# Optimization experiments

Measured on AMD Instinct MI355X. Metric: run time of the kernel, lower is better.

## Reference

```python
import jax, jax.numpy as jnp
import numpy as np
import math

N_HEADS = 12


def setup_inputs() -> dict:
    key = jax.random.key(0)
    ks = jax.random.split(key, 6)
    B, S, DIM = 4, 2048, 768
    h = jax.random.normal(ks[0], (B, S, DIM), dtype=jnp.float32)
    attn_mask = jnp.ones((B, 1, 1, S), dtype=jnp.int32)
    scale = 1.0 / math.sqrt(DIM)
    wq = jax.random.normal(ks[1], (DIM, DIM), dtype=jnp.float32) * scale
    wk = jax.random.normal(ks[2], (DIM, DIM), dtype=jnp.float32) * scale
    wv = jax.random.normal(ks[3], (DIM, DIM), dtype=jnp.float32) * scale
    wo = jax.random.normal(ks[4], (DIM, DIM), dtype=jnp.float32) * scale
    return {"h": h, "attn_mask": attn_mask, "wq": wq, "wk": wk, "wv": wv, "wo": wo}


def reference(h, attn_mask, wq, wk, wv, wo):
    B, S, dim = h.shape
    H = N_HEADS
    D = dim // H
    qk_scale = 1.0 / math.sqrt(D)
    # NOTE: original uses .view(B, H, S, D) on the [B, S, H*D] projection —
    # a raw reshape, NOT the usual (B,S,H,D)->(B,H,S,D) transpose. Reproduce exactly.
    hq = (h @ wq.T).reshape(B, H, S, D)
    hk = (h @ wk.T).reshape(B, H, S, D)
    hv = (h @ wv.T).reshape(B, H, S, D)
    scores = jnp.einsum("bhqd,bhkd->bhqk", hq, hk) * qk_scale  # [B,H,S,S]
    scores = jnp.where(attn_mask == 0, -jnp.inf, scores)
    attn = jax.nn.softmax(scores.astype(jnp.float32), axis=-1)
    ctx = jnp.einsum("bhqk,bhkd->bhqd", attn, hv)  # [B,H,S,D]
    # dropout is identity in eval mode
    ctx = ctx.reshape(B, S, H * D)
    return ctx @ wo.T
```

## Files before the change

### kernel.cpp

```cpp
#include <hip/hip_runtime.h>
#include <math.h>

typedef __bf16 bf16x8 __attribute__((ext_vector_type(8)));
typedef float  f32x4  __attribute__((ext_vector_type(4)));
typedef float  f32x16 __attribute__((ext_vector_type(16)));

#define MFMA16(a, b, c) __builtin_amdgcn_mfma_f32_16x16x32_bf16((a), (b), (c), 0, 0, 0)
#define MFMA32(a, b, c) __builtin_amdgcn_mfma_f32_32x32x16_bf16((a), (b), (c), 0, 0, 0)

__device__ __forceinline__ unsigned short f2bf(float f) {
    unsigned int u = __float_as_uint(f);
    u += 0x7fffu + ((u >> 16) & 1u);
    return (unsigned short)(u >> 16);
}

__device__ __forceinline__ void gll16(const unsigned short* g, unsigned short* l) {
    __builtin_amdgcn_global_load_lds(
        (const __attribute__((address_space(1))) unsigned int*)g,
        (__attribute__((address_space(3))) unsigned int*)l, 16, 0, 0);
}

__global__ __launch_bounds__(256) void convert_kernel(
    const float* __restrict__ h, const float* __restrict__ wq,
    const float* __restrict__ wk, const float* __restrict__ wv,
    const float* __restrict__ wo,
    unsigned short* __restrict__ hb, unsigned short* __restrict__ wb)
{
    const int NH4 = 1572864;
    const int NW4 = 147456;
    int i4 = blockIdx.x * 256 + threadIdx.x;
    const float4* src;
    unsigned short* dst;
    int off;
    float sc = 1.0f;
    if (i4 < NH4) {
        src = (const float4*)h; dst = hb; off = i4;
    } else {
        int j = i4 - NH4;
        int w = j / NW4;
        off = j - w * NW4;
        const float* s = (w == 0) ? wq : (w == 1) ? wk : (w == 2) ? wv : wo;
        if (w == 0) sc = 0.18033688011112042f;
        src = (const float4*)s;
        dst = wb + w * 589824;
    }
    float4 v = src[off];
    ushort4 o;
    o.x = f2bf(v.x * sc); o.y = f2bf(v.y * sc);
    o.z = f2bf(v.z * sc); o.w = f2bf(v.w * sc);
    ((ushort4*)dst)[off] = o;
}

template <typename OutT>
__global__ __launch_bounds__(256) void gemm_bt(
    const unsigned short* __restrict__ A,
    const unsigned short* __restrict__ Bm,
    OutT* __restrict__ C)
{
    constexpr int K = 768, N = 768;
    __shared__ unsigned short As[2][128 * 32];
    __shared__ unsigned short Bs[2][128 * 32];
    const unsigned short* Bz = Bm + (size_t)blockIdx.z * N * K;
    OutT* Cz = C + (size_t)blockIdx.z * 8192 * N;

    const int tid  = threadIdx.x;
    const int bm   = blockIdx.x * 128, bn = blockIdx.y * 128;
    const int wave = tid >> 6, lane = tid & 63;
    const int wm   = (wave & 1) * 64, wn = (wave >> 1) * 64;
    const int l16  = lane & 15, quad = lane >> 4;

    const int sr  = tid >> 2;
    const int sp8 = ((tid & 3) ^ (sr & 3)) * 8;
    const int slot8 = (quad ^ (l16 & 3)) * 8;

    auto stage = [&](int k0, int bi) {
        gll16(A  + (size_t)(bm + sr) * K      + k0 + sp8, As[bi] + tid * 8);
        gll16(A  + (size_t)(bm + 64 + sr) * K + k0 + sp8, As[bi] + 2048 + tid * 8);
        gll16(Bz + (size_t)(bn + sr) * K      + k0 + sp8, Bs[bi] + tid * 8);
        gll16(Bz + (size_t)(bn + 64 + sr) * K + k0 + sp8, Bs[bi] + 2048 + tid * 8);
    };

    f32x4 acc[4][4] = {};

    stage(0, 0);
    __syncthreads();

    for (int i = 0; i < 24; i++) {
        const int cur = i & 1;
        if (i < 23) stage((i + 1) * 32, cur ^ 1);

        bf16x8 af[4], bfv[4];
        #pragma unroll
        for (int ii = 0; ii < 4; ii++)
            af[ii] = *(const bf16x8*)(As[cur] + (wm + ii * 16 + l16) * 32 + slot8);
        #pragma unroll
        for (int jj = 0; jj < 4; jj++)
            bfv[jj] = *(const bf16x8*)(Bs[cur] + (wn + jj * 16 + l16) * 32 + slot8);
        #pragma unroll
        for (int ii = 0; ii < 4; ii++)
            #pragma unroll
            for (int jj = 0; jj < 4; jj++)
                acc[ii][jj] = MFMA16(af[ii], bfv[jj], acc[ii][jj]);

        __syncthreads();
    }

    #pragma unroll
    for (int ii = 0; ii < 4; ii++) {
        #pragma unroll
        for (int jj = 0; jj < 4; jj++) {
            int row0 = bm + wm + ii * 16 + quad * 4;
            int col  = bn + wn + jj * 16 + l16;
            #pragma unroll
            for (int r = 0; r < 4; r++) {
                float v = acc[ii][jj][r];
                size_t idx = (size_t)(row0 + r) * N + col;
                if constexpr (sizeof(OutT) == 2) Cz[idx] = f2bf(v);
                else                             Cz[idx] = v;
            }
        }
    }
}

__global__ __launch_bounds__(256) void vtrans_kernel(
    const unsigned short* __restrict__ Vg,
    unsigned short* __restrict__ vt)
{
    constexpr int LDT = 72;
    __shared__ unsigned short Ts[64 * LDT];
    const int b = blockIdx.z, hh = blockIdx.y, kp0 = blockIdx.x * 64;
    const int tid = threadIdx.x;
    const size_t boff = (size_t)b * (24576 * 64);
    const int rowV0 = hh * 2048 + kp0;

    #pragma unroll
    for (int rep = 0; rep < 2; rep++) {
        int idx = rep * 256 + tid;
        int r = idx >> 3, dp = (idx & 7) * 8;
        uint4 v = *(const uint4*)(Vg + boff + (size_t)(rowV0 + r) * 64 + dp);
        unsigned short tmp[8];
        *(uint4*)tmp = v;
        #pragma unroll
        for (int i = 0; i < 8; i++) Ts[(dp + i) * LDT + r] = tmp[i];
    }
    __syncthreads();
    unsigned short* vtb = vt + ((size_t)(b * 12 + hh)) * 64 * 2048;
    #pragma unroll
    for (int rep = 0; rep < 2; rep++) {
        int idx = rep * 256 + tid;
        int d = idx >> 3, kp = (idx & 7) * 8;
        uint4 v = *(const uint4*)(Ts + d * LDT + kp);
        *(uint4*)(vtb + (size_t)d * 2048 + kp0 + kp) = v;
    }
}

__global__ __launch_bounds__(256) void attn_kernel(
    const unsigned short* __restrict__ Qg,
    const unsigned short* __restrict__ Kg,
    const unsigned short* __restrict__ vt,
    const int* __restrict__ mask,
    unsigned short* __restrict__ Og)
{
    __shared__ unsigned short Ks[3 * 2048];
    __shared__ unsigned short Vs[3 * 2048];
    __shared__ unsigned long long msh[32];

    const int b = blockIdx.z, hh = blockIdx.y, qt = blockIdx.x;
    const int tid  = threadIdx.x;
    const int wave = tid >> 6, lane = tid & 63;
    const int c31  = lane & 31, h = lane >> 5;
    const size_t boff = (size_t)b * (24576 * 64);
    const int rowQ0 = hh * 2048 + qt * 128;
    const int rowK0 = hh * 2048;
    const unsigned short* vtg = vt + ((size_t)(b * 12 + hh)) * 64 * 2048;
    const int swk = c31 & 7;
    const int swv = c31 & 3;

    const int srowK = tid >> 3;
    const int schK  = ((tid & 7) ^ (srowK & 7)) * 8;
    const int srowV = tid >> 2;
    const int schV  = ((tid & 3) ^ (srowV & 3)) * 8;

    auto stageKV = [&](int kt, int bi) {
        gll16(Kg  + boff + (size_t)(rowK0 + kt * 32 + srowK) * 64 + schK,
              Ks + bi * 2048 + tid * 8);
        gll16(vtg + (size_t)srowV * 2048 + kt * 32 + schV,
              Vs + bi * 2048 + tid * 8);
    };

    bf16x8 qf[4];
    {
        const unsigned short* qrow =
            Qg + boff + (size_t)(rowQ0 + wave * 32 + c31) * 64;
        #pragma unroll
        for (int c = 0; c < 4; c++)
            qf[c] = *(const bf16x8*)(qrow + (2 * c + h) * 8);
    }

    {
        const int4 a = *(const int4*)(mask + b * 2048 + tid * 8);
        const int4 c = *(const int4*)(mask + b * 2048 + tid * 8 + 4);
        unsigned char byte =
            (a.x != 0 ? 1u : 0u)       | (a.y != 0 ? 2u : 0u) |
            (a.z != 0 ? 4u : 0u)       | (a.w != 0 ? 8u : 0u) |
            (c.x != 0 ? 16u : 0u)      | (c.y != 0 ? 32u : 0u) |
            (c.z != 0 ? 64u : 0u)      | (c.w != 0 ? 128u : 0u);
        ((unsigned char*)msh)[tid] = byte;
    }
    __syncthreads();

    stageKV(0, 0);
    stageKV(1, 1);

    f32x16 acc[2] = {};
    f32x16 acc_l  = {};
    bf16x8 onesf;
    #pragma unroll
    for (int i = 0; i < 8; i++) onesf[i] = (__bf16)1.0f;

    int cur = 0;
    for (int kt = 0; kt < 64; kt++) {
        if (kt < 63) asm volatile("s_waitcnt vmcnt(2)\n\ts_barrier" ::: "memory");
        else         asm volatile("s_waitcnt vmcnt(0)\n\ts_barrier" ::: "memory");
        __builtin_amdgcn_sched_barrier(0);

        if (kt < 62) {
            int nb = cur + 2; if (nb >= 3) nb -= 3;
            stageKV(kt + 2, nb);
        }

        const unsigned int am = ((const unsigned int*)msh)[kt];
        const unsigned short* Kc = Ks + cur * 2048;
        const unsigned short* Vc = Vs + cur * 2048;

        f32x16 sT;
        {
            f32x16 z = {};
            __builtin_amdgcn_s_setprio(1);
            #pragma unroll
            for (int c = 0; c < 4; c++) {
                int ch = (2 * c + h) ^ swk;
                bf16x8 kf = *(const bf16x8*)(Kc + c31 * 64 + ch * 8);
                z = MFMA32(kf, qf[c], z);
            }
            __builtin_amdgcn_s_setprio(0);
            sT = z;
        }

        unsigned int p01[4], p23[4];
        if (am == 0xFFFFFFFFu) {
            #pragma unroll
            for (int s = 0; s < 4; s++) {
                float e0 = __builtin_amdgcn_exp2f(sT[4*s+0]);
                float e1 = __builtin_amdgcn_exp2f(sT[4*s+1]);
                float e2 = __builtin_amdgcn_exp2f(sT[4*s+2]);
                float e3 = __builtin_amdgcn_exp2f(sT[4*s+3]);
                asm("v_cvt_pk_bf16_f32 %0, %1, %2"
                    : "=v"(p01[s]) : "v"(e0), "v"(e1));
                asm("v_cvt_pk_bf16_f32 %0, %1, %2"
                    : "=v"(p23[s]) : "v"(e2), "v"(e3));
            }
        } else {
            #pragma unroll
            for (int s = 0; s < 4; s++) {
                unsigned int nib = (am >> (8 * s + 4 * h)) & 0xFu;
                float e0 = __builtin_amdgcn_exp2f(sT[4*s+0]);
                float e1 = __builtin_amdgcn_exp2f(sT[4*s+1]);
                float e2 = __builtin_amdgcn_exp2f(sT[4*s+2]);
                float e3 = __builtin_amdgcn_exp2f(sT[4*s+3]);
                e0 = (nib & 1u) ? e0 : 0.f;
                e1 = (nib & 2u) ? e1 : 0.f;
                e2 = (nib & 4u) ? e2 : 0.f;
                e3 = (nib & 8u) ? e3 : 0.f;
                asm("v_cvt_pk_bf16_f32 %0, %1, %2"
                    : "=v"(p01[s]) : "v"(e0), "v"(e1));
                asm("v_cvt_pk_bf16_f32 %0, %1, %2"
                    : "=v"(p23[s]) : "v"(e2), "v"(e3));
            }
        }

        __builtin_amdgcn_s_setprio(1);
        #pragma unroll
        for (int kc = 0; kc < 2; kc++) {
            unsigned int a01 = p01[2 * kc], b01 = p01[2 * kc + 1];
            unsigned int a23 = p23[2 * kc], b23 = p23[2 * kc + 1];
            asm("v_permlane32_swap_b32 %0, %1" : "+v"(a01), "+v"(b01));
            asm("v_permlane32_swap_b32 %0, %1" : "+v"(a23), "+v"(b23));
            uint4 pfu;
            pfu.x = a01;
            pfu.y = a23;
            pfu.z = b01;
            pfu.w = b23;
            bf16x8 pf;
            __builtin_memcpy(&pf, &pfu, 16);
            #pragma unroll
            for (int nt = 0; nt < 2; nt++) {
                int chv = (2 * kc + h) ^ swv;
                bf16x8 vf = *(const bf16x8*)(Vc + (nt * 32 + c31) * 32 + chv * 8);
                acc[nt] = MFMA32(pf, vf, acc[nt]);
            }
            acc_l = MFMA32(pf, onesf, acc_l);
        }
        __builtin_amdgcn_s_setprio(0);

        cur = (cur == 2) ? 0 : cur + 1;
    }

    #pragma unroll
    for (int reg = 0; reg < 16; reg++) {
        int rowfn = (reg & 3) + 8 * (reg >> 2) + 4 * h;
        float li = __builtin_amdgcn_rcpf(acc_l[reg]);
        int row = rowQ0 + wave * 32 + rowfn;
        #pragma unroll
        for (int nt = 0; nt < 2; nt++)
            Og[boff + (size_t)row * 64 + nt * 32 + c31] = f2bf(acc[nt][reg] * li);
    }
}

extern "C" void kernel_launch(void* const* d_in, const int* in_sizes, int n_in,
                              void* d_out, int out_size, void* d_ws, size_t ws_size,
                              hipStream_t stream)
{
    const float* h    = (const float*)d_in[0];
    const int*   mask = (const int*)d_in[1];
    const float* wq   = (const float*)d_in[2];
    const float* wk   = (const float*)d_in[3];
    const float* wv   = (const float*)d_in[4];
    const float* wo   = (const float*)d_in[5];

    unsigned short* hb  = (unsigned short*)d_ws;
    unsigned short* wb  = hb + 6291456;
    unsigned short* qkv = wb + 4 * 589824;
    unsigned short* ctx = qkv + (size_t)3 * 6291456;

    convert_kernel<<<8448, 256, 0, stream>>>(h, wq, wk, wv, wo, hb, wb);
    gemm_bt<unsigned short><<<dim3(64, 6, 3), 256, 0, stream>>>(hb, wb, qkv);
    vtrans_kernel<<<dim3(32, 12, 4), 256, 0, stream>>>(qkv + (size_t)2 * 6291456, hb);
    attn_kernel<<<dim3(16, 12, 4), 256, 0, stream>>>(
        qkv, qkv + 6291456, hb, mask, ctx);
    gemm_bt<float><<<dim3(64, 6, 1), 256, 0, stream>>>(
        ctx, wb + (size_t)3 * 589824, (float*)d_out);
}
```

Measured before the change: 244.3 us.

## Split attention key range across two blocks and combine partials; tweak LDS swizzle

The attention kernel is templated on a key-split factor. With SPLIT=2, each (batch, head, query-tile) is handled by two blocks, each covering half of the key tiles. Each block writes unnormalized fp32 partial outputs and row sums, and a new combine kernel adds them, normalizes and converts to bf16. This doubles the grid to give the GPU more parallel work. The cost is an extra kernel launch and a large fp32 round trip through global memory. The LDS swizzle for K and V is also changed to XOR in higher row bits, which is meant to cut bank conflicts. The split path runs only when the workspace is large enough, otherwise the original single-pass path is used.

```diff
diff --git a/kernel.cpp b/kernel.cpp
--- a/kernel.cpp
+++ b/kernel.cpp
@@ -154,18 +154,25 @@
     }
 }
 
+template <int SPLIT>
 __global__ __launch_bounds__(256) void attn_kernel(
     const unsigned short* __restrict__ Qg,
     const unsigned short* __restrict__ Kg,
     const unsigned short* __restrict__ vt,
     const int* __restrict__ mask,
-    unsigned short* __restrict__ Og)
+    unsigned short* __restrict__ Og,
+    float* __restrict__ Op,
+    float* __restrict__ lp)
 {
     __shared__ unsigned short Ks[3 * 2048];
     __shared__ unsigned short Vs[3 * 2048];
     __shared__ unsigned long long msh[32];
 
-    const int b = blockIdx.z, hh = blockIdx.y, qt = blockIdx.x;
+    constexpr int NT = 64 / SPLIT;
+    const int z = blockIdx.z;
+    const int b = z / SPLIT, kz = z % SPLIT;
+    const int ktbase = kz * NT;
+    const int hh = blockIdx.y, qt = blockIdx.x;
     const int tid  = threadIdx.x;
     const int wave = tid >> 6, lane = tid & 63;
     const int c31  = lane & 31, h = lane >> 5;
@@ -173,13 +180,13 @@
     const int rowQ0 = hh * 2048 + qt * 128;
     const int rowK0 = hh * 2048;
     const unsigned short* vtg = vt + ((size_t)(b * 12 + hh)) * 64 * 2048;
-    const int swk = c31 & 7;
-    const int swv = c31 & 3;
+    const int swk = (c31 & 7) ^ (c31 >> 3);
+    const int swv = (c31 & 3) ^ ((c31 >> 2) & 3);
 
     const int srowK = tid >> 3;
-    const int schK  = ((tid & 7) ^ (srowK & 7)) * 8;
+    const int schK  = ((tid & 7) ^ (srowK & 7) ^ ((srowK >> 3) & 3)) * 8;
     const int srowV = tid >> 2;
-    const int schV  = ((tid & 3) ^ (srowV & 3)) * 8;
+    const int schV  = ((tid & 3) ^ (srowV & 3) ^ ((srowV >> 2) & 3)) * 8;
 
     auto stageKV = [&](int kt, int bi) {
         gll16(Kg  + boff + (size_t)(rowK0 + kt * 32 + srowK) * 64 + schK,
@@ -209,8 +216,8 @@
     }
     __syncthreads();
 
-    stageKV(0, 0);
-    stageKV(1, 1);
+    stageKV(ktbase + 0, 0);
+    stageKV(ktbase + 1, 1);
 
     f32x16 acc[2] = {};
     f32x16 acc_l  = {};
@@ -219,12 +226,13 @@
     for (int i = 0; i < 8; i++) onesf[i] = (__bf16)1.0f;
 
     int cur = 0;
-    for (int kt = 0; kt < 64; kt++) {
-        if (kt < 63) asm volatile("s_waitcnt vmcnt(2)\n\ts_barrier" ::: "memory");
-        else         asm volatile("s_waitcnt vmcnt(0)\n\ts_barrier" ::: "memory");
+    for (int lt = 0; lt < NT; lt++) {
+        const int kt = ktbase + lt;
+        if (lt < NT - 1) asm volatile("s_waitcnt vmcnt(2)\n\ts_barrier" ::: "memory");
+        else             asm volatile("s_waitcnt vmcnt(0)\n\ts_barrier" ::: "memory");
         __builtin_amdgcn_sched_barrier(0);
 
-        if (kt < 62) {
+        if (lt < NT - 2) {
             int nb = cur + 2; if (nb >= 3) nb -= 3;
             stageKV(kt + 2, nb);
         }
@@ -235,16 +243,16 @@
 
         f32x16 sT;
         {
-            f32x16 z = {};
+            f32x16 z2 = {};
             __builtin_amdgcn_s_setprio(1);
             #pragma unroll
             for (int c = 0; c < 4; c++) {
                 int ch = (2 * c + h) ^ swk;
                 bf16x8 kf = *(const bf16x8*)(Kc + c31 * 64 + ch * 8);
-                z = MFMA32(kf, qf[c], z);
+                z2 = MFMA32(kf, qf[c], z2);
             }
             __builtin_amdgcn_s_setprio(0);
-            sT = z;
+            sT = z2;
         }
 
         unsigned int p01[4], p23[4];
@@ -306,15 +314,50 @@
         cur = (cur == 2) ? 0 : cur + 1;
     }
 
-    #pragma unroll
-    for (int reg = 0; reg < 16; reg++) {
-        int rowfn = (reg & 3) + 8 * (reg >> 2) + 4 * h;
-        float li = __builtin_amdgcn_rcpf(acc_l[reg]);
-        int row = rowQ0 + wave * 32 + rowfn;
-        #pragma unroll
-        for (int nt = 0; nt < 2; nt++)
-            Og[boff + (size_t)row * 64 + nt * 32 + c31] = f2bf(acc[nt][reg] * li);
-    }
+    if constexpr (SPLIT == 1) {
+        #pragma unroll
+        for (int reg = 0; reg < 16; reg++) {
+            int rowfn = (reg & 3) + 8 * (reg >> 2) + 4 * h;
+            float li = __builtin_amdgcn_rcpf(acc_l[reg]);
+            int row = rowQ0 + wave * 32 + rowfn;
+            #pragma unroll
+            for (int nt = 0; nt < 2; nt++)
+                Og[boff + (size_t)row * 64 + nt * 32 + c31] = f2bf(acc[nt][reg] * li);
+        }
+    } else {
+        float* Opz = Op + (size_t)kz * 6291456 + boff;
+        float* lpz = lp + (size_t)kz * 98304 + b * 24576;
+        #pragma unroll
+        for (int reg = 0; reg < 16; reg++) {
+            int rowfn = (reg & 3) + 8 * (reg >> 2) + 4 * h;
+            int row = rowQ0 + wave * 32 + rowfn;
+            #pragma unroll
+            for (int nt = 0; nt < 2; nt++)
+                Opz[(size_t)row * 64 + nt * 32 + c31] = acc[nt][reg];
+            if (c31 == 0) lpz[row] = acc_l[reg];
+        }
+    }
+}
+
+__global__ __launch_bounds__(256) void combine_kernel(
+    const float* __restrict__ Op,
+    const float* __restrict__ lp,
+    unsigned short* __restrict__ ctx)
+{
+    const size_t idx8 = ((size_t)blockIdx.x * 256 + threadIdx.x) * 8;
+    const int row = (int)(idx8 >> 6);
+    const float linv = __builtin_amdgcn_rcpf(lp[row] + lp[98304 + row]);
+    const float4 a0 = *(const float4*)(Op + idx8);
+    const float4 a1 = *(const float4*)(Op + idx8 + 4);
+    const float4 b0 = *(const float4*)(Op + 6291456 + idx8);
+    const float4 b1 = *(const float4*)(Op + 6291456 + idx8 + 4);
+    ushort4 o0, o1;
+    o0.x = f2bf((a0.x + b0.x) * linv); o0.y = f2bf((a0.y + b0.y) * linv);
+    o0.z = f2bf((a0.z + b0.z) * linv); o0.w = f2bf((a0.w + b0.w) * linv);
+    o1.x = f2bf((a1.x + b1.x) * linv); o1.y = f2bf((a1.y + b1.y) * linv);
+    o1.z = f2bf((a1.z + b1.z) * linv); o1.w = f2bf((a1.w + b1.w) * linv);
+    *(ushort4*)(ctx + idx8)     = o0;
+    *(ushort4*)(ctx + idx8 + 4) = o1;
 }
 
 extern "C" void kernel_launch(void* const* d_in, const int* in_sizes, int n_in,
@@ -332,12 +375,23 @@
     unsigned short* wb  = hb + 6291456;
     unsigned short* qkv = wb + 4 * 589824;
     unsigned short* ctx = qkv + (size_t)3 * 6291456;
+    float* Op = (float*)(ctx + 6291456);
+    float* lp = Op + (size_t)2 * 6291456;
+    const size_t ws_need = 33816576ull * 2
+                         + (2ull * 6291456 + 2ull * 98304) * 4;
+    const bool split = ws_size >= ws_need;
 
     convert_kernel<<<8448, 256, 0, stream>>>(h, wq, wk, wv, wo, hb, wb);
     gemm_bt<unsigned short><<<dim3(64, 6, 3), 256, 0, stream>>>(hb, wb, qkv);
     vtrans_kernel<<<dim3(32, 12, 4), 256, 0, stream>>>(qkv + (size_t)2 * 6291456, hb);
-    attn_kernel<<<dim3(16, 12, 4), 256, 0, stream>>>(
-        qkv, qkv + 6291456, hb, mask, ctx);
+    if (split) {
+        attn_kernel<2><<<dim3(16, 12, 8), 256, 0, stream>>>(
+            qkv, qkv + 6291456, hb, mask, ctx, Op, lp);
+        combine_kernel<<<3072, 256, 0, stream>>>(Op, lp, ctx);
+    } else {
+        attn_kernel<1><<<dim3(16, 12, 4), 256, 0, stream>>>(
+            qkv, qkv + 6291456, hb, mask, ctx, nullptr, nullptr);
+    }
     gemm_bt<float><<<dim3(64, 6, 1), 256, 0, stream>>>(
         ctx, wb + (size_t)3 * 589824, (float*)d_out);
 }
```

Measured after the change: 254.2 us. 4.0% more time.

## Triple-buffer GEMM loads, remap workgroups across XCDs, reswizzle attention LDS

Applied to the files above, without the earlier changes.

The projection GEMM goes from a double-buffered LDS pipeline with two __syncthreads per step to a three-stage ring. Each step issues a prefetch two tiles ahead and waits with a partial vmcnt before a single barrier. Workgroups now use a 1D grid remapped so consecutive tiles land on the same XCD, for better L2 reuse of shared A/B tiles. The attention kernel's K/V LDS XOR swizzle also mixes in higher row bits to reduce bank conflicts. In exchange, LDS use in the GEMM rises by half, and the swizzle has to stay consistent between the stores and the reads.

```diff
diff --git a/kernel.cpp b/kernel.cpp
--- a/kernel.cpp
+++ b/kernel.cpp
@@ -58,13 +58,21 @@
     OutT* __restrict__ C)
 {
     constexpr int K = 768, N = 768;
-    __shared__ unsigned short As[2][128 * 32];
-    __shared__ unsigned short Bs[2][128 * 32];
-    const unsigned short* Bz = Bm + (size_t)blockIdx.z * N * K;
-    OutT* Cz = C + (size_t)blockIdx.z * 8192 * N;
+    __shared__ unsigned short As[3][128 * 32];
+    __shared__ unsigned short Bs[3][128 * 32];
+
+    const int nwg  = gridDim.x;
+    const int orig = blockIdx.x;
+    const int lid  = (orig & 7) * (nwg >> 3) + (orig >> 3);
+    const int nx   = lid % 6;
+    const int t    = lid / 6;
+    const int bm   = (t & 63) * 128, bn = nx * 128;
+    const int bz   = t >> 6;
+
+    const unsigned short* Bz = Bm + (size_t)bz * N * K;
+    OutT* Cz = C + (size_t)bz * 8192 * N;
 
     const int tid  = threadIdx.x;
-    const int bm   = blockIdx.x * 128, bn = blockIdx.y * 128;
     const int wave = tid >> 6, lane = tid & 63;
     const int wm   = (wave & 1) * 64, wn = (wave >> 1) * 64;
     const int l16  = lane & 15, quad = lane >> 4;
@@ -83,11 +91,18 @@
     f32x4 acc[4][4] = {};
 
     stage(0, 0);
-    __syncthreads();
-
+    stage(32, 1);
+
+    int cur = 0;
     for (int i = 0; i < 24; i++) {
-        const int cur = i & 1;
-        if (i < 23) stage((i + 1) * 32, cur ^ 1);
+        if (i < 23) asm volatile("s_waitcnt vmcnt(4)\n\ts_barrier" ::: "memory");
+        else        asm volatile("s_waitcnt vmcnt(0)\n\ts_barrier" ::: "memory");
+        __builtin_amdgcn_sched_barrier(0);
+
+        if (i < 22) {
+            int nb = cur + 2; if (nb >= 3) nb -= 3;
+            stage((i + 2) * 32, nb);
+        }
 
         bf16x8 af[4], bfv[4];
         #pragma unroll
@@ -102,7 +117,7 @@
             for (int jj = 0; jj < 4; jj++)
                 acc[ii][jj] = MFMA16(af[ii], bfv[jj], acc[ii][jj]);
 
-        __syncthreads();
+        cur = (cur == 2) ? 0 : cur + 1;
     }
 
     #pragma unroll
@@ -173,13 +188,13 @@
     const int rowQ0 = hh * 2048 + qt * 128;
     const int rowK0 = hh * 2048;
     const unsigned short* vtg = vt + ((size_t)(b * 12 + hh)) * 64 * 2048;
-    const int swk = c31 & 7;
-    const int swv = c31 & 3;
+    const int swk = (c31 & 7) ^ (c31 >> 3);
+    const int swv = (c31 & 3) ^ ((c31 >> 2) & 3);
 
     const int srowK = tid >> 3;
-    const int schK  = ((tid & 7) ^ (srowK & 7)) * 8;
+    const int schK  = ((tid & 7) ^ (srowK & 7) ^ ((srowK >> 3) & 3)) * 8;
     const int srowV = tid >> 2;
-    const int schV  = ((tid & 3) ^ (srowV & 3)) * 8;
+    const int schV  = ((tid & 3) ^ (srowV & 3) ^ ((srowV >> 2) & 3)) * 8;
 
     auto stageKV = [&](int kt, int bi) {
         gll16(Kg  + boff + (size_t)(rowK0 + kt * 32 + srowK) * 64 + schK,
@@ -235,16 +250,16 @@
 
         f32x16 sT;
         {
-            f32x16 z = {};
+            f32x16 z2 = {};
             __builtin_amdgcn_s_setprio(1);
             #pragma unroll
             for (int c = 0; c < 4; c++) {
                 int ch = (2 * c + h) ^ swk;
                 bf16x8 kf = *(const bf16x8*)(Kc + c31 * 64 + ch * 8);
-                z = MFMA32(kf, qf[c], z);
+                z2 = MFMA32(kf, qf[c], z2);
             }
             __builtin_amdgcn_s_setprio(0);
-            sT = z;
+            sT = z2;
         }
 
         unsigned int p01[4], p23[4];
@@ -334,10 +349,10 @@
     unsigned short* ctx = qkv + (size_t)3 * 6291456;
 
     convert_kernel<<<8448, 256, 0, stream>>>(h, wq, wk, wv, wo, hb, wb);
-    gemm_bt<unsigned short><<<dim3(64, 6, 3), 256, 0, stream>>>(hb, wb, qkv);
+    gemm_bt<unsigned short><<<1152, 256, 0, stream>>>(hb, wb, qkv);
     vtrans_kernel<<<dim3(32, 12, 4), 256, 0, stream>>>(qkv + (size_t)2 * 6291456, hb);
     attn_kernel<<<dim3(16, 12, 4), 256, 0, stream>>>(
         qkv, qkv + 6291456, hb, mask, ctx);
-    gemm_bt<float><<<dim3(64, 6, 1), 256, 0, stream>>>(
+    gemm_bt<float><<<384, 256, 0, stream>>>(
         ctx, wb + (size_t)3 * 589824, (float*)d_out);
 }
```

Measured after the change: 239.8 us. About the same (-1.8%).
